# Performance work log

Hardware: AMD Instinct MI355X
Metric: run time of the kernel (lower is better)

The kernel has to match this reference:

```python
import jax, jax.numpy as jnp
import numpy as np

B, T = 32, 64
INPUT_DIM, EMB, HA, HB, NUM_CLASS = 4894, 128, 128, 128, 1
D_IN = EMB + 1  # use_time=True appends scalar time feature


def gru_cell(x, h, Wih, Whh, bih, bhh):
    # torch nn.GRU cell semantics, gate order (r, z, n)
    gi = x @ Wih.T + bih
    gh = h @ Whh.T + bhh
    ir, iz, i_n = jnp.split(gi, 3, axis=-1)
    hr, hz, hn = jnp.split(gh, 3, axis=-1)
    r = jax.nn.sigmoid(ir + hr)
    z = jax.nn.sigmoid(iz + hz)
    n = jnp.tanh(i_n + r * hn)
    return (1.0 - z) * n + z * h


def setup_inputs():
    key = jax.random.key(0)
    ks = jax.random.split(key, 14)
    f32 = jnp.float32
    s = lambda k, sh, sc: (jax.random.normal(k, sh) * sc).astype(f32)
    return {
        "x": jax.random.uniform(ks[0], (B, T, INPUT_DIM), dtype=f32),
        "t": jax.random.uniform(ks[1], (B, T), dtype=f32),
        "lengths": jax.random.randint(ks[2], (B,), 1, T + 1),
        "W_emb": s(ks[3], (EMB, INPUT_DIM), 0.02),
        "Wih_a": s(ks[4], (3 * HA, D_IN), 0.05),
        "Whh_a": s(ks[5], (3 * HA, HA), 0.05),
        "bih_a": jnp.zeros((3 * HA,), f32),
        "bhh_a": jnp.zeros((3 * HA,), f32),
        "Wih_b": s(ks[6], (3 * HB, D_IN), 0.05),
        "Whh_b": s(ks[7], (3 * HB, HB), 0.05),
        "bih_b": jnp.zeros((3 * HB,), f32),
        "bhh_b": jnp.zeros((3 * HB,), f32),
        "w_alpha": s(ks[8], (1, HA), 0.1),
        "b_alpha": jnp.zeros((1,), f32),
        "W_beta": s(ks[9], (EMB, HB), 0.1),
        "b_beta": jnp.zeros((EMB,), f32),
        "W_out": s(ks[10], (NUM_CLASS, EMB), 0.1),
        "b_out": jnp.zeros((NUM_CLASS,), f32),
    }


def reference(x, t, lengths, W_emb, Wih_a, Whh_a, bih_a, bhh_a,
              Wih_b, Whh_b, bih_b, bhh_b, w_alpha, b_alpha,
              W_beta, b_beta, W_out, b_out):
    # embedding (dropout is identity in inference)
    emb = x @ W_emb.T                                   # [B,T,E]
    temb = jnp.concatenate([emb, t[..., None]], axis=-1)  # [B,T,E+1]

    # reversed-prefix tensor: R[b,i,k] = temb[b, i-k] for k<=i else 0
    i_idx = jnp.arange(T)[:, None]
    k_idx = jnp.arange(T)[None, :]
    src = i_idx - k_idx                                  # [T,T]
    valid = (src >= 0)
    src_c = jnp.clip(src, 0)
    vmask = valid[None, :, :, None].astype(emb.dtype)
    R = jnp.take(temb, src_c, axis=1) * vmask            # [B,T,T,D_IN]
    E_rev = jnp.take(emb, src_c, axis=1) * vmask         # [B,T,T,E]

    # run alpha/beta GRUs along the prefix axis k (causal, so zero padding
    # at k>i never affects the k<=i outputs that we keep)
    R_k = jnp.moveaxis(R, 2, 0)                          # [Tk,B,T,D_IN]
    h0a = jnp.zeros((B, T, HA), emb.dtype)
    h0b = jnp.zeros((B, T, HB), emb.dtype)

    def step(carry, xk):
        ha, hb = carry
        ha = gru_cell(xk, ha, Wih_a, Whh_a, bih_a, bhh_a)
        hb = gru_cell(xk, hb, Wih_b, Whh_b, bih_b, bhh_b)
        return (ha, hb), (ha, hb)

    _, (Ha, Hb) = jax.lax.scan(step, (h0a, h0b), R_k)
    Ha = jnp.moveaxis(Ha, 0, 2)                          # [B,T,Tk,HA]
    Hb = jnp.moveaxis(Hb, 0, 2)                          # [B,T,Tk,HB]

    # attention over the i+1 prefix positions
    scores = (Ha @ w_alpha.T + b_alpha)[..., 0]          # [B,T,Tk]
    scores = jnp.where(valid[None], scores, jnp.float32(-1e9))
    alpha = jax.nn.softmax(scores, axis=-1)
    beta = jnp.tanh(Hb @ W_beta.T + b_beta)              # [B,T,Tk,E]

    c = jnp.einsum('btk,btke,btke->bte', alpha, beta, E_rev)
    row_valid = (jnp.arange(T)[None, :] < lengths[:, None]).astype(c.dtype)
    c = c * row_valid[..., None]                         # zero where i >= lengths[b]

    logits = c @ W_out.T + b_out                         # [B,T,1]
    return logits[..., 0]
```

## Files before the change

### kernel.cpp

```cpp
#include <hip/hip_runtime.h>
#include <hip/hip_bf16.h>

#define DEVI __device__ __forceinline__

typedef __attribute__((ext_vector_type(8))) short short8;
typedef __attribute__((ext_vector_type(8))) unsigned short ushort8;
typedef __attribute__((ext_vector_type(2))) unsigned int u32x2;
typedef __attribute__((ext_vector_type(4))) float f32x4;

static constexpr int TT = 64, KIN = 4894, KINP = 4896, E = 128;
static constexpr float L2E = 1.4426950408889634f;

DEVI unsigned short f2bf(float f) {
    union { float f; unsigned u; } v; v.f = f;
    unsigned r = v.u + 0x7fffu + ((v.u >> 16) & 1u);
    return (unsigned short)(r >> 16);
}
DEVI float sigm2(float x) { return __builtin_amdgcn_rcpf(1.f + __builtin_amdgcn_exp2f(-x)); }
DEVI float tanh2(float x) { return 1.f - 2.f * __builtin_amdgcn_rcpf(__builtin_amdgcn_exp2f(x + x) + 1.f); }

DEVI void gload16(const float* g, float* l) {
    __builtin_amdgcn_global_load_lds(
        (const __attribute__((address_space(1))) void*)g,
        (__attribute__((address_space(3))) void*)l, 16, 0, 0);
}

DEVI short8 cvt8(const float* __restrict__ p, float s) {
    float2 v0 = *(const float2*)p, v1 = *(const float2*)(p + 2);
    float2 v2 = *(const float2*)(p + 4), v3 = *(const float2*)(p + 6);
    short8 r;
    r[0] = (short)f2bf(v0.x * s); r[1] = (short)f2bf(v0.y * s);
    r[2] = (short)f2bf(v1.x * s); r[3] = (short)f2bf(v1.y * s);
    r[4] = (short)f2bf(v2.x * s); r[5] = (short)f2bf(v2.y * s);
    r[6] = (short)f2bf(v3.x * s); r[7] = (short)f2bf(v3.y * s);
    return r;
}
DEVI short8 cvt8pk(const float* __restrict__ p) {
    float2 v0 = *(const float2*)p, v1 = *(const float2*)(p + 2);
    float2 v2 = *(const float2*)(p + 4), v3 = *(const float2*)(p + 6);
    union { unsigned u[4]; short8 s; } o;
    asm("v_cvt_pk_bf16_f32 %0, %1, %2" : "=v"(o.u[0]) : "v"(v0.x), "v"(v0.y));
    asm("v_cvt_pk_bf16_f32 %0, %1, %2" : "=v"(o.u[1]) : "v"(v1.x), "v"(v1.y));
    asm("v_cvt_pk_bf16_f32 %0, %1, %2" : "=v"(o.u[2]) : "v"(v2.x), "v"(v2.y));
    asm("v_cvt_pk_bf16_f32 %0, %1, %2" : "=v"(o.u[3]) : "v"(v3.x), "v"(v3.y));
    return o.s;
}

__global__ void prep_kernel(const float* __restrict__ Wemb,
                            const float* __restrict__ Wih_a, const float* __restrict__ Wih_b,
                            const float* __restrict__ Whh_a, const float* __restrict__ Whh_b,
                            const float* __restrict__ Wbeta,
                            unsigned short* __restrict__ wembbf, unsigned short* __restrict__ wihbf,
                            unsigned short* __restrict__ whhbf, unsigned short* __restrict__ wbetabf) {
    int job = blockIdx.x * blockDim.x + threadIdx.x;
    const int JWE = 128 * 612, JWIH = 768 * 16, JWHH = 768 * 16, JWB = 128 * 16;
    if (job < JWE) {
        int row = job / 612, c8 = (job % 612) * 8;
        ushort8 v;
        #pragma unroll
        for (int jj = 0; jj < 8; ++jj) { int c = c8 + jj; v[jj] = (c < KIN) ? f2bf(Wemb[(long)row * KIN + c]) : (unsigned short)0; }
        *(ushort8*)(wembbf + (long)row * KINP + c8) = v;
        return;
    }
    job -= JWE;
    if (job < JWIH) {
        int g = job / 16, c8 = (job % 16) * 8;
        const float* src = (g < 384) ? (Wih_a + (long)g * 129) : (Wih_b + (long)(g - 384) * 129);
        ushort8 v;
        #pragma unroll
        for (int jj = 0; jj < 8; ++jj) v[jj] = f2bf(src[c8 + jj] * L2E);
        *(ushort8*)(wihbf + (long)g * 128 + c8) = v;
        return;
    }
    job -= JWIH;
    if (job < JWHH) {
        int g = job / 16, c8 = (job % 16) * 8;
        const float* src = (g < 384) ? (Whh_a + (long)g * 128) : (Whh_b + (long)(g - 384) * 128);
        ushort8 v;
        #pragma unroll
        for (int jj = 0; jj < 8; ++jj) v[jj] = f2bf(src[c8 + jj] * L2E);
        *(ushort8*)(whhbf + (long)g * 128 + c8) = v;
        return;
    }
    job -= JWHH;
    if (job < JWB) {
        int e = job / 16, c8 = (job % 16) * 8;
        ushort8 v;
        #pragma unroll
        for (int jj = 0; jj < 8; ++jj) v[jj] = f2bf(Wbeta[(long)e * 128 + c8 + jj] * L2E);
        *(ushort8*)(wbetabf + (long)e * 128 + c8) = v;
    }
}

__global__ __launch_bounds__(256) void emb_gemm(const float* __restrict__ x,
                                                const unsigned short* __restrict__ wembbf,
                                                float* __restrict__ pout) {
    const int ks = blockIdx.x & 3, m0 = (blockIdx.x >> 2) * 16;
    const int w = threadIdx.x >> 6, l = threadIdx.x & 63, lr = l & 15, lo = l >> 4;
    const int n0 = (2 * w) * 16 + lr, n1 = (2 * w + 1) * 16 + lr;
    const float* xrow = x + (long)(m0 + lr) * KIN;
    const int k0 = ks * 1216;
    f32x4 acc0 = {0, 0, 0, 0}, acc1 = {0, 0, 0, 0};
    #pragma unroll 2
    for (int kt = 0; kt < 38; ++kt) {
        int k = k0 + kt * 32 + lo * 8;
        short8 a = cvt8pk(xrow + k);
        short8 b0 = *(const short8*)(wembbf + (long)n0 * KINP + k);
        short8 b1 = *(const short8*)(wembbf + (long)n1 * KINP + k);
        acc0 = __builtin_amdgcn_mfma_f32_16x16x32_bf16(a, b0, acc0, 0, 0, 0);
        acc1 = __builtin_amdgcn_mfma_f32_16x16x32_bf16(a, b1, acc1, 0, 0, 0);
    }
    if (ks == 3) {
        int k = 4864 + lo * 8;
        short8 a;
        #pragma unroll
        for (int jj = 0; jj < 8; ++jj) { int c = k + jj; a[jj] = (c < KIN) ? (short)f2bf(xrow[c]) : (short)0; }
        short8 b0 = *(const short8*)(wembbf + (long)n0 * KINP + k);
        short8 b1 = *(const short8*)(wembbf + (long)n1 * KINP + k);
        acc0 = __builtin_amdgcn_mfma_f32_16x16x32_bf16(a, b0, acc0, 0, 0, 0);
        acc1 = __builtin_amdgcn_mfma_f32_16x16x32_bf16(a, b1, acc1, 0, 0, 0);
    }
    float* pbase = pout + (long)ks * 2048 * E;
    #pragma unroll
    for (int r = 0; r < 4; ++r) {
        int m = m0 + lo * 4 + r;
        pbase[(long)m * E + n0] = acc0[r];
        pbase[(long)m * E + n1] = acc1[r];
    }
}

__global__ __launch_bounds__(256) void gi_gemm(const float* __restrict__ pout,
                                               const unsigned short* __restrict__ wihbf,
                                               const float* __restrict__ Wih_a, const float* __restrict__ Wih_b,
                                               const float* __restrict__ t,
                                               const float* __restrict__ bih_a, const float* __restrict__ bih_b,
                                               const float* __restrict__ bhh_a, const float* __restrict__ bhh_b,
                                               const float* __restrict__ Wout,
                                               float* __restrict__ emb_swz_wo, float* __restrict__ Gi3) {
    const int m0 = blockIdx.x * 16;
    const int tid = threadIdx.x;
    const int w = tid >> 6, l = tid & 63, lr = l & 15, lo = l >> 4;
    __shared__ __align__(16) unsigned short embs[16][128];

    {
        const int trow = tid >> 4, e0 = (tid & 15) * 8;
        const int tok = m0 + trow;
        const long base = (long)tok * E + e0;
        f32x4 s0 = *(const f32x4*)(pout + base);
        f32x4 s1 = *(const f32x4*)(pout + base + 4);
        #pragma unroll
        for (int ks = 1; ks < 4; ++ks) {
            f32x4 v0 = *(const f32x4*)(pout + (long)ks * 2048 * E + base);
            f32x4 v1 = *(const f32x4*)(pout + (long)ks * 2048 * E + base + 4);
            #pragma unroll
            for (int jj = 0; jj < 4; ++jj) { s0[jj] += v0[jj]; s1[jj] += v1[jj]; }
        }
        ushort8 h;
        #pragma unroll
        for (int jj = 0; jj < 4; ++jj) { h[jj] = f2bf(s0[jj]); h[4 + jj] = f2bf(s1[jj]); }
        *(ushort8*)(&embs[trow][e0]) = h;
        f32x4 wo0 = *(const f32x4*)(Wout + e0);
        f32x4 wo1 = *(const f32x4*)(Wout + e0 + 4);
        #pragma unroll
        for (int jj = 0; jj < 4; ++jj) { s0[jj] *= wo0[jj]; s1[jj] *= wo1[jj]; }
        const int cc = (tok >> 6) & 15;
        const int x0 = e0 ^ ((cc & 7) << 2), x1 = (e0 + 4) ^ ((cc & 7) << 2);
        *(f32x4*)(emb_swz_wo + (long)tok * E + x0) = s0;
        *(f32x4*)(emb_swz_wo + (long)tok * E + x1) = s1;
    }
    __syncthreads();

    f32x4 acc[12];
    #pragma unroll
    for (int nl = 0; nl < 12; ++nl) acc[nl] = (f32x4){0, 0, 0, 0};
    #pragma unroll
    for (int kt = 0; kt < 4; ++kt) {
        int k = kt * 32 + lo * 8;
        short8 a0 = *(const short8*)(&embs[lr][k]);
        #pragma unroll
        for (int nl = 0; nl < 12; ++nl) {
            int n = (w * 12 + nl) * 16 + lr;
            short8 bf = *(const short8*)(wihbf + (long)n * 128 + k);
            acc[nl] = __builtin_amdgcn_mfma_f32_16x16x32_bf16(a0, bf, acc[nl], 0, 0, 0);
        }
    }
    #pragma unroll
    for (int nl = 0; nl < 12; ++nl) {
        int n = (w * 12 + nl) * 16 + lr;
        int gru = (n >= 384) ? 1 : 0;
        int nn = n - gru * 384;
        int gt = nn >> 7, u = nn & 127;
        float bias = (gru ? bih_b[nn] : bih_a[nn]);
        if (gt < 2) bias += (gru ? bhh_b[nn] : bhh_a[nn]);
        float cw = (n < 384) ? Wih_a[(long)n * 129 + 128] : Wih_b[(long)(n - 384) * 129 + 128];
        #pragma unroll
        for (int r = 0; r < 4; ++r) {
            int tok = m0 + lo * 4 + r;
            int cc = (tok >> 6) & 15;
            Gi3[(((long)tok * 2 + gru) * 3 + gt) * 128 + (u ^ ((cc & 7) << 2))] =
                acc[nl][r] + (bias + t[tok] * cw) * L2E;
        }
    }
}

__global__ __launch_bounds__(512, 1)
void retain_rec(const unsigned short* __restrict__ whhbf, const unsigned short* __restrict__ wbetabf,
                const float* __restrict__ Gi3, const float* __restrict__ emb_swz_wo,
                const float* __restrict__ bhh_a, const float* __restrict__ bhh_b,
                const float* __restrict__ w_alpha, const float* __restrict__ b_alpha,
                const float* __restrict__ b_beta,
                float* __restrict__ p_g, float* __restrict__ d_g) {
    const int tid = threadIdx.x;
    const int w = tid >> 6, l = tid & 63, lr = l & 15, lo = l >> 4;
    const int i = blockIdx.x >> 2, q = (blockIdx.x >> 1) & 1, g = blockIdx.x & 1;
    const int u0 = w * 16 + lo * 4;
    const int sw2 = (lr & 7) << 2;
    const int cS = tid >> 5, chk = tid & 31;

    __shared__ __align__(16) float Gst[3][3][16][128];
    __shared__ __align__(16) float Est[3][16][128];
    __shared__ __align__(16) unsigned short Hbf[2][16][128];
    __shared__ __align__(16) unsigned short Mld[2][16][128];
    __shared__ float pd_s[16][66];

    for (int idx = tid; idx < 2 * 16 * 128; idx += 512) (&Hbf[0][0][0])[idx] = 0;

    short8 Wf[3][4];
    #pragma unroll
    for (int gt = 0; gt < 3; ++gt)
        #pragma unroll
        for (int kt = 0; kt < 4; ++kt)
            Wf[gt][kt] = *(const short8*)(whhbf + (long)(g * 384 + gt * 128 + w * 16 + lr) * 128 + kt * 32 + lo * 8);
    short8 Xf[4];
    #pragma unroll
    for (int kt = 0; kt < 4; ++kt)
        Xf[kt] = g ? *(const short8*)(wbetabf + (long)(w * 16 + lr) * 128 + kt * 32 + lo * 8)
                   : cvt8(w_alpha + kt * 32 + lo * 8, L2E);
    short8 ones;
    #pragma unroll
    for (int jj = 0; jj < 8; ++jj) ones[jj] = (short)0x3F80;

    const float* bhhG = g ? bhh_b : bhh_a;
    f32x4 bhn4 = *(const f32x4*)(bhhG + 256 + u0);
    #pragma unroll
    for (int r = 0; r < 4; ++r) bhn4[r] *= L2E;
    f32x4 bb4 = {0, 0, 0, 0};
    if (g) {
        bb4 = *(const f32x4*)(b_beta + u0);
        #pragma unroll
        for (int r = 0; r < 4; ++r) bb4[r] *= L2E;
    }
    const float balL = b_alpha[0] * L2E;

    float h_old[4] = {0, 0, 0, 0};

    const long chainBase = (long)((q * 16 + cS) * 64);
    auto STAGE = [&](int b, int jg, int je) {
        const float* gb = Gi3 + ((chainBase + jg) * 2 + g) * 384 + chk * 4;
        gload16(gb,        (float*)&Gst[b][0][0][0] + (w << 8));
        gload16(gb + 128,  (float*)&Gst[b][1][0][0] + (w << 8));
        gload16(gb + 256,  (float*)&Gst[b][2][0][0] + (w << 8));
        if (g) gload16(emb_swz_wo + ((chainBase + je) << 7) + chk * 4, (float*)&Est[b][0][0] + (w << 8));
    };

    STAGE(0, i, (i + 1 > 63) ? 63 : i + 1);
    STAGE(1, (i - 1 < 0) ? 0 : i - 1, i);
    if (g) asm volatile("s_waitcnt lgkmcnt(0) vmcnt(4)" ::: "memory");
    else   asm volatile("s_waitcnt lgkmcnt(0) vmcnt(3)" ::: "memory");
    __builtin_amdgcn_s_barrier();
    __builtin_amdgcn_sched_barrier(0);

    const int iend = i + 1 + g;
    for (int n = 0; n <= iend; ++n) {
        const int bufc = n % 3, bufs = (n + 2) % 3;
        const int rb = n & 1, wb = rb ^ 1;
        const bool do_gate = (n <= i);
        const bool do_post = (n >= 1) && (n <= i + 1);

        {
            int jg = i - n - 2; if (jg < 0) jg = 0;
            int je = i - n - 1; if (je < 0) je = 0;
            STAGE(bufs, jg, je);
        }

        if (g && w == 0 && n >= 2) {
            f32x4 dacc = {0, 0, 0, 0};
            #pragma unroll
            for (int kt = 0; kt < 4; ++kt) {
                int sw = (kt * 32 + lo * 8) ^ ((lr & 7) * 8);
                short8 bm = *(const short8*)(&Mld[wb][lr][sw]);
                dacc = __builtin_amdgcn_mfma_f32_16x16x32_bf16(ones, bm, dacc, 0, 0, 0);
            }
            if (lo == 0) pd_s[lr][n - 2] = dacc[0];
        }

        short8 Af[4];
        if (do_gate || do_post) {
            #pragma unroll
            for (int kt = 0; kt < 4; ++kt) {
                int sw = (kt * 32 + lo * 8) ^ ((lr & 7) * 8);
                Af[kt] = *(const short8*)(&Hbf[rb][lr][sw]);
            }
        }

        f32x4 gh0 = {0, 0, 0, 0}, gh1 = {0, 0, 0, 0}, gh2 = bhn4;
        if (do_gate) {
            f32x4 a0 = {0, 0, 0, 0}, a1 = {0, 0, 0, 0}, a2 = {0, 0, 0, 0};
            #pragma unroll
            for (int kt = 0; kt < 2; ++kt) {
                gh0 = __builtin_amdgcn_mfma_f32_16x16x32_bf16(Wf[0][kt], Af[kt], gh0, 0, 0, 0);
                gh1 = __builtin_amdgcn_mfma_f32_16x16x32_bf16(Wf[1][kt], Af[kt], gh1, 0, 0, 0);
                gh2 = __builtin_amdgcn_mfma_f32_16x16x32_bf16(Wf[2][kt], Af[kt], gh2, 0, 0, 0);
                a0 = __builtin_amdgcn_mfma_f32_16x16x32_bf16(Wf[0][kt + 2], Af[kt + 2], a0, 0, 0, 0);
                a1 = __builtin_amdgcn_mfma_f32_16x16x32_bf16(Wf[1][kt + 2], Af[kt + 2], a1, 0, 0, 0);
                a2 = __builtin_amdgcn_mfma_f32_16x16x32_bf16(Wf[2][kt + 2], Af[kt + 2], a2, 0, 0, 0);
            }
            #pragma unroll
            for (int r = 0; r < 4; ++r) { gh0[r] += a0[r]; gh1[r] += a1[r]; gh2[r] += a2[r]; }
        }

        if (do_post) {
            f32x4 xacc = {0, 0, 0, 0}, xb = {0, 0, 0, 0};
            #pragma unroll
            for (int kt = 0; kt < 2; ++kt) {
                xacc = __builtin_amdgcn_mfma_f32_16x16x32_bf16(Xf[kt], Af[kt], xacc, 0, 0, 0);
                xb   = __builtin_amdgcn_mfma_f32_16x16x32_bf16(Xf[kt + 2], Af[kt + 2], xb, 0, 0, 0);
            }
            #pragma unroll
            for (int r = 0; r < 4; ++r) xacc[r] += xb[r];
            if (!g) {
                if (w == 0 && lo == 0) pd_s[lr][n - 1] = __builtin_amdgcn_exp2f(xacc[0] + balL);
            } else {
                f32x4 ew4 = *(const f32x4*)(&Est[bufc][lr][u0 ^ sw2]);
                float m0v = tanh2(xacc[0] + bb4[0]) * ew4[0];
                float m1v = tanh2(xacc[1] + bb4[1]) * ew4[1];
                float m2v = tanh2(xacc[2] + bb4[2]) * ew4[2];
                float m3v = tanh2(xacc[3] + bb4[3]) * ew4[3];
                unsigned mp0, mp1;
                asm("v_cvt_pk_bf16_f32 %0, %1, %2" : "=v"(mp0) : "v"(m0v), "v"(m1v));
                asm("v_cvt_pk_bf16_f32 %0, %1, %2" : "=v"(mp1) : "v"(m2v), "v"(m3v));
                *(u32x2*)(&Mld[rb][lr][u0 ^ ((lr & 7) * 8)]) = (u32x2){mp0, mp1};
            }
        }

        if (do_gate) {
            f32x4 gr = *(const f32x4*)(&Gst[bufc][0][lr][u0 ^ sw2]);
            f32x4 gz = *(const f32x4*)(&Gst[bufc][1][lr][u0 ^ sw2]);
            f32x4 gn = *(const f32x4*)(&Gst[bufc][2][lr][u0 ^ sw2]);
            float hn[4];
            #pragma unroll
            for (int r = 0; r < 4; ++r) {
                float rr = sigm2(gr[r] + gh0[r]);
                float zz = sigm2(gz[r] + gh1[r]);
                float nv = tanh2(gn[r] + rr * gh2[r]);
                float h = nv + zz * (h_old[r] - nv);
                h_old[r] = h;
                hn[r] = h;
            }
            unsigned p0, p1;
            asm("v_cvt_pk_bf16_f32 %0, %1, %2" : "=v"(p0) : "v"(hn[0]), "v"(hn[1]));
            asm("v_cvt_pk_bf16_f32 %0, %1, %2" : "=v"(p1) : "v"(hn[2]), "v"(hn[3]));
            *(u32x2*)(&Hbf[wb][lr][u0 ^ ((lr & 7) * 8)]) = (u32x2){p0, p1};
        }

        if (g) asm volatile("s_waitcnt lgkmcnt(0) vmcnt(4)" ::: "memory");
        else   asm volatile("s_waitcnt lgkmcnt(0) vmcnt(3)" ::: "memory");
        __builtin_amdgcn_s_barrier();
        __builtin_amdgcn_sched_barrier(0);
    }

    __syncthreads();

    float* dst = g ? d_g : p_g;
    for (int idx = tid; idx < 16 * 64; idx += 512) {
        int c = idx >> 6, kk = idx & 63;
        if (kk <= i) {
            long row = (long)(q * 16 + c) * 64 + i;
            dst[row * 64 + kk] = pd_s[c][kk];
        }
    }
}

__global__ __launch_bounds__(512) void reduce_out(const float* __restrict__ p_g, const float* __restrict__ d_g,
                                                  const int* __restrict__ lengths, const float* __restrict__ b_out,
                                                  float* __restrict__ out) {
    const int w = threadIdx.x >> 6, l = threadIdx.x & 63;
    const int row = blockIdx.x * 8 + w;
    const int b = row >> 6, i = row & 63;
    float p = (l <= i) ? p_g[(long)row * 64 + l] : 0.f;
    float d = (l <= i) ? d_g[(long)row * 64 + l] : 0.f;
    float pd = p * d;
    #pragma unroll
    for (int off = 1; off < 64; off <<= 1) {
        p += __shfl_xor(p, off);
        pd += __shfl_xor(pd, off);
    }
    if (l == 0) {
        float val = (i < lengths[b]) ? pd / p + b_out[0] : b_out[0];
        out[row] = val;
    }
}

extern "C" void kernel_launch(void* const* d_in, const int* in_sizes, int n_in,
                              void* d_out, int out_size, void* d_ws, size_t ws_size,
                              hipStream_t stream) {
    (void)in_sizes; (void)n_in; (void)out_size; (void)ws_size;
    const float* x       = (const float*)d_in[0];
    const float* t       = (const float*)d_in[1];
    const int*   len     = (const int*)d_in[2];
    const float* Wemb    = (const float*)d_in[3];
    const float* Wih_a   = (const float*)d_in[4];
    const float* Whh_a   = (const float*)d_in[5];
    const float* bih_a   = (const float*)d_in[6];
    const float* bhh_a   = (const float*)d_in[7];
    const float* Wih_b   = (const float*)d_in[8];
    const float* Whh_b   = (const float*)d_in[9];
    const float* bih_b   = (const float*)d_in[10];
    const float* bhh_b   = (const float*)d_in[11];
    const float* w_alpha = (const float*)d_in[12];
    const float* b_alpha = (const float*)d_in[13];
    const float* W_beta  = (const float*)d_in[14];
    const float* b_beta  = (const float*)d_in[15];
    const float* W_out   = (const float*)d_in[16];
    const float* b_out   = (const float*)d_in[17];

    char* ws = (char*)d_ws;
    float*          emb_swz = (float*)(ws + 0);
    float*          Gi3     = (float*)(ws + 1048576);
    unsigned short* wembbf  = (unsigned short*)(ws + 7340032);
    unsigned short* wihbf   = (unsigned short*)(ws + 8593408);
    unsigned short* whhbf   = (unsigned short*)(ws + 8790016);
    unsigned short* wbetabf = (unsigned short*)(ws + 8986624);
    float*          p_g     = (float*)(ws + 9019392);
    float*          d_g     = (float*)(ws + 9543680);
    float*          pout    = (float*)(ws + 10067968);

    const int jobs = 128 * 612 + 768 * 16 + 768 * 16 + 128 * 16;
    prep_kernel<<<(jobs + 255) / 256, 256, 0, stream>>>(Wemb, Wih_a, Wih_b, Whh_a, Whh_b, W_beta,
                                                        wembbf, wihbf, whhbf, wbetabf);
    emb_gemm<<<512, 256, 0, stream>>>(x, wembbf, pout);
    gi_gemm<<<128, 256, 0, stream>>>(pout, wihbf, Wih_a, Wih_b, t, bih_a, bih_b, bhh_a, bhh_b,
                                     W_out, emb_swz, Gi3);
    retain_rec<<<256, 512, 0, stream>>>(whhbf, wbetabf, Gi3, emb_swz, bhh_a, bhh_b,
                                        w_alpha, b_alpha, b_beta, p_g, d_g);
    reduce_out<<<256, 512, 0, stream>>>(p_g, d_g, len, b_out, (float*)d_out);
}
```

Measured before the change: 134.4 us.

## Halve recurrence block to 4 waves, double-buffer staging, and deepen emb split-K

```diff
diff --git a/kernel.cpp b/kernel.cpp
--- a/kernel.cpp
+++ b/kernel.cpp
@@ -95,14 +95,14 @@
 __global__ __launch_bounds__(256) void emb_gemm(const float* __restrict__ x,
                                                 const unsigned short* __restrict__ wembbf,
                                                 float* __restrict__ pout) {
-    const int ks = blockIdx.x & 3, m0 = (blockIdx.x >> 2) * 16;
+    const int ks = blockIdx.x & 7, m0 = (blockIdx.x >> 3) * 16;
     const int w = threadIdx.x >> 6, l = threadIdx.x & 63, lr = l & 15, lo = l >> 4;
     const int n0 = (2 * w) * 16 + lr, n1 = (2 * w + 1) * 16 + lr;
     const float* xrow = x + (long)(m0 + lr) * KIN;
-    const int k0 = ks * 1216;
+    const int k0 = ks * 608;
     f32x4 acc0 = {0, 0, 0, 0}, acc1 = {0, 0, 0, 0};
     #pragma unroll 2
-    for (int kt = 0; kt < 38; ++kt) {
+    for (int kt = 0; kt < 19; ++kt) {
         int k = k0 + kt * 32 + lo * 8;
         short8 a = cvt8pk(xrow + k);
         short8 b0 = *(const short8*)(wembbf + (long)n0 * KINP + k);
@@ -110,7 +110,7 @@
         acc0 = __builtin_amdgcn_mfma_f32_16x16x32_bf16(a, b0, acc0, 0, 0, 0);
         acc1 = __builtin_amdgcn_mfma_f32_16x16x32_bf16(a, b1, acc1, 0, 0, 0);
     }
-    if (ks == 3) {
+    if (ks == 7) {
         int k = 4864 + lo * 8;
         short8 a;
         #pragma unroll
@@ -149,7 +149,7 @@
         f32x4 s0 = *(const f32x4*)(pout + base);
         f32x4 s1 = *(const f32x4*)(pout + base + 4);
         #pragma unroll
-        for (int ks = 1; ks < 4; ++ks) {
+        for (int ks = 1; ks < 8; ++ks) {
             f32x4 v0 = *(const f32x4*)(pout + (long)ks * 2048 * E + base);
             f32x4 v1 = *(const f32x4*)(pout + (long)ks * 2048 * E + base + 4);
             #pragma unroll
@@ -203,7 +203,7 @@
     }
 }
 
-__global__ __launch_bounds__(512, 1)
+__global__ __launch_bounds__(256, 1)
 void retain_rec(const unsigned short* __restrict__ whhbf, const unsigned short* __restrict__ wbetabf,
                 const float* __restrict__ Gi3, const float* __restrict__ emb_swz_wo,
                 const float* __restrict__ bhh_a, const float* __restrict__ bhh_b,
@@ -213,81 +213,89 @@
     const int tid = threadIdx.x;
     const int w = tid >> 6, l = tid & 63, lr = l & 15, lo = l >> 4;
     const int i = blockIdx.x >> 2, q = (blockIdx.x >> 1) & 1, g = blockIdx.x & 1;
-    const int u0 = w * 16 + lo * 4;
+    const int u0a = w * 32 + lo * 4, u0b = u0a + 16;
     const int sw2 = (lr & 7) << 2;
+    const int bsw = (lr & 7) * 8;
     const int cS = tid >> 5, chk = tid & 31;
 
-    __shared__ __align__(16) float Gst[3][3][16][128];
-    __shared__ __align__(16) float Est[3][16][128];
+    __shared__ __align__(16) float Gst[2][3][16][128];
+    __shared__ __align__(16) float Est[2][16][128];
     __shared__ __align__(16) unsigned short Hbf[2][16][128];
     __shared__ __align__(16) unsigned short Mld[2][16][128];
     __shared__ float pd_s[16][66];
 
-    for (int idx = tid; idx < 2 * 16 * 128; idx += 512) (&Hbf[0][0][0])[idx] = 0;
-
-    short8 Wf[3][4];
-    #pragma unroll
-    for (int gt = 0; gt < 3; ++gt)
+    for (int idx = tid; idx < 2 * 16 * 128; idx += 256) (&Hbf[0][0][0])[idx] = 0;
+
+    short8 Wf[6][4];
+    #pragma unroll
+    for (int ut = 0; ut < 2; ++ut)
+        #pragma unroll
+        for (int gt = 0; gt < 3; ++gt)
+            #pragma unroll
+            for (int kt = 0; kt < 4; ++kt)
+                Wf[ut * 3 + gt][kt] = *(const short8*)(whhbf +
+                    (long)(g * 384 + gt * 128 + w * 32 + ut * 16 + lr) * 128 + kt * 32 + lo * 8);
+    short8 Xf[2][4];
+    #pragma unroll
+    for (int ut = 0; ut < 2; ++ut)
         #pragma unroll
         for (int kt = 0; kt < 4; ++kt)
-            Wf[gt][kt] = *(const short8*)(whhbf + (long)(g * 384 + gt * 128 + w * 16 + lr) * 128 + kt * 32 + lo * 8);
-    short8 Xf[4];
-    #pragma unroll
-    for (int kt = 0; kt < 4; ++kt)
-        Xf[kt] = g ? *(const short8*)(wbetabf + (long)(w * 16 + lr) * 128 + kt * 32 + lo * 8)
-                   : cvt8(w_alpha + kt * 32 + lo * 8, L2E);
+            Xf[ut][kt] = g ? *(const short8*)(wbetabf + (long)(w * 32 + ut * 16 + lr) * 128 + kt * 32 + lo * 8)
+                           : cvt8(w_alpha + kt * 32 + lo * 8, L2E);
     short8 ones;
     #pragma unroll
     for (int jj = 0; jj < 8; ++jj) ones[jj] = (short)0x3F80;
 
     const float* bhhG = g ? bhh_b : bhh_a;
-    f32x4 bhn4 = *(const f32x4*)(bhhG + 256 + u0);
-    #pragma unroll
-    for (int r = 0; r < 4; ++r) bhn4[r] *= L2E;
-    f32x4 bb4 = {0, 0, 0, 0};
+    f32x4 bhn4a = *(const f32x4*)(bhhG + 256 + u0a);
+    f32x4 bhn4b = *(const f32x4*)(bhhG + 256 + u0b);
+    #pragma unroll
+    for (int r = 0; r < 4; ++r) { bhn4a[r] *= L2E; bhn4b[r] *= L2E; }
+    f32x4 bb4a = {0, 0, 0, 0}, bb4b = {0, 0, 0, 0};
     if (g) {
-        bb4 = *(const f32x4*)(b_beta + u0);
-        #pragma unroll
-        for (int r = 0; r < 4; ++r) bb4[r] *= L2E;
+        bb4a = *(const f32x4*)(b_beta + u0a);
+        bb4b = *(const f32x4*)(b_beta + u0b);
+        #pragma unroll
+        for (int r = 0; r < 4; ++r) { bb4a[r] *= L2E; bb4b[r] *= L2E; }
     }
     const float balL = b_alpha[0] * L2E;
 
-    float h_old[4] = {0, 0, 0, 0};
-
-    const long chainBase = (long)((q * 16 + cS) * 64);
+    float h_old[2][4] = {{0, 0, 0, 0}, {0, 0, 0, 0}};
+
     auto STAGE = [&](int b, int jg, int je) {
-        const float* gb = Gi3 + ((chainBase + jg) * 2 + g) * 384 + chk * 4;
-        gload16(gb,        (float*)&Gst[b][0][0][0] + (w << 8));
-        gload16(gb + 128,  (float*)&Gst[b][1][0][0] + (w << 8));
-        gload16(gb + 256,  (float*)&Gst[b][2][0][0] + (w << 8));
-        if (g) gload16(emb_swz_wo + ((chainBase + je) << 7) + chk * 4, (float*)&Est[b][0][0] + (w << 8));
+        #pragma unroll
+        for (int h = 0; h < 2; ++h) {
+            const long cb = (long)((q * 16 + cS + 8 * h) * 64);
+            const float* gb = Gi3 + ((cb + jg) * 2 + g) * 384 + chk * 4;
+            const int dofs = (w << 8) + (h << 10);
+            gload16(gb,       (float*)&Gst[b][0][0][0] + dofs);
+            gload16(gb + 128, (float*)&Gst[b][1][0][0] + dofs);
+            gload16(gb + 256, (float*)&Gst[b][2][0][0] + dofs);
+            if (g) gload16(emb_swz_wo + ((cb + je) << 7) + chk * 4, (float*)&Est[b][0][0] + dofs);
+        }
     };
 
     STAGE(0, i, (i + 1 > 63) ? 63 : i + 1);
-    STAGE(1, (i - 1 < 0) ? 0 : i - 1, i);
-    if (g) asm volatile("s_waitcnt lgkmcnt(0) vmcnt(4)" ::: "memory");
-    else   asm volatile("s_waitcnt lgkmcnt(0) vmcnt(3)" ::: "memory");
-    __builtin_amdgcn_s_barrier();
-    __builtin_amdgcn_sched_barrier(0);
 
     const int iend = i + 1 + g;
     for (int n = 0; n <= iend; ++n) {
-        const int bufc = n % 3, bufs = (n + 2) % 3;
-        const int rb = n & 1, wb = rb ^ 1;
+        __syncthreads();
+
+        {
+            int jg = i - n - 1; if (jg < 0) jg = 0;
+            int je = i - n;     if (je < 0) je = 0;
+            STAGE((n + 1) & 1, jg, je);
+        }
+
+        const int rb = n & 1, wb = rb ^ 1, bufc = n & 1;
         const bool do_gate = (n <= i);
         const bool do_post = (n >= 1) && (n <= i + 1);
 
-        {
-            int jg = i - n - 2; if (jg < 0) jg = 0;
-            int je = i - n - 1; if (je < 0) je = 0;
-            STAGE(bufs, jg, je);
-        }
-
         if (g && w == 0 && n >= 2) {
             f32x4 dacc = {0, 0, 0, 0};
             #pragma unroll
             for (int kt = 0; kt < 4; ++kt) {
-                int sw = (kt * 32 + lo * 8) ^ ((lr & 7) * 8);
+                int sw = (kt * 32 + lo * 8) ^ bsw;
                 short8 bm = *(const short8*)(&Mld[wb][lr][sw]);
                 dacc = __builtin_amdgcn_mfma_f32_16x16x32_bf16(ones, bm, dacc, 0, 0, 0);
             }
@@ -298,81 +306,90 @@
         if (do_gate || do_post) {
             #pragma unroll
             for (int kt = 0; kt < 4; ++kt) {
-                int sw = (kt * 32 + lo * 8) ^ ((lr & 7) * 8);
+                int sw = (kt * 32 + lo * 8) ^ bsw;
                 Af[kt] = *(const short8*)(&Hbf[rb][lr][sw]);
             }
         }
 
-        f32x4 gh0 = {0, 0, 0, 0}, gh1 = {0, 0, 0, 0}, gh2 = bhn4;
+        f32x4 gh[6];
+        gh[0] = (f32x4){0, 0, 0, 0}; gh[1] = (f32x4){0, 0, 0, 0}; gh[2] = bhn4a;
+        gh[3] = (f32x4){0, 0, 0, 0}; gh[4] = (f32x4){0, 0, 0, 0}; gh[5] = bhn4b;
         if (do_gate) {
-            f32x4 a0 = {0, 0, 0, 0}, a1 = {0, 0, 0, 0}, a2 = {0, 0, 0, 0};
-            #pragma unroll
-            for (int kt = 0; kt < 2; ++kt) {
-                gh0 = __builtin_amdgcn_mfma_f32_16x16x32_bf16(Wf[0][kt], Af[kt], gh0, 0, 0, 0);
-                gh1 = __builtin_amdgcn_mfma_f32_16x16x32_bf16(Wf[1][kt], Af[kt], gh1, 0, 0, 0);
-                gh2 = __builtin_amdgcn_mfma_f32_16x16x32_bf16(Wf[2][kt], Af[kt], gh2, 0, 0, 0);
-                a0 = __builtin_amdgcn_mfma_f32_16x16x32_bf16(Wf[0][kt + 2], Af[kt + 2], a0, 0, 0, 0);
-                a1 = __builtin_amdgcn_mfma_f32_16x16x32_bf16(Wf[1][kt + 2], Af[kt + 2], a1, 0, 0, 0);
-                a2 = __builtin_amdgcn_mfma_f32_16x16x32_bf16(Wf[2][kt + 2], Af[kt + 2], a2, 0, 0, 0);
-            }
-            #pragma unroll
-            for (int r = 0; r < 4; ++r) { gh0[r] += a0[r]; gh1[r] += a1[r]; gh2[r] += a2[r]; }
+            #pragma unroll
+            for (int kt = 0; kt < 4; ++kt)
+                #pragma unroll
+                for (int tt = 0; tt < 6; ++tt)
+                    gh[tt] = __builtin_amdgcn_mfma_f32_16x16x32_bf16(Wf[tt][kt], Af[kt], gh[tt], 0, 0, 0);
         }
 
         if (do_post) {
-            f32x4 xacc = {0, 0, 0, 0}, xb = {0, 0, 0, 0};
-            #pragma unroll
-            for (int kt = 0; kt < 2; ++kt) {
-                xacc = __builtin_amdgcn_mfma_f32_16x16x32_bf16(Xf[kt], Af[kt], xacc, 0, 0, 0);
-                xb   = __builtin_amdgcn_mfma_f32_16x16x32_bf16(Xf[kt + 2], Af[kt + 2], xb, 0, 0, 0);
-            }
-            #pragma unroll
-            for (int r = 0; r < 4; ++r) xacc[r] += xb[r];
             if (!g) {
-                if (w == 0 && lo == 0) pd_s[lr][n - 1] = __builtin_amdgcn_exp2f(xacc[0] + balL);
+                if (w == 0) {
+                    f32x4 xacc = {0, 0, 0, 0};
+                    #pragma unroll
+                    for (int kt = 0; kt < 4; ++kt)
+                        xacc = __builtin_amdgcn_mfma_f32_16x16x32_bf16(Xf[0][kt], Af[kt], xacc, 0, 0, 0);
+                    if (lo == 0) pd_s[lr][n - 1] = __builtin_amdgcn_exp2f(xacc[0] + balL);
+                }
             } else {
-                f32x4 ew4 = *(const f32x4*)(&Est[bufc][lr][u0 ^ sw2]);
-                float m0v = tanh2(xacc[0] + bb4[0]) * ew4[0];
-                float m1v = tanh2(xacc[1] + bb4[1]) * ew4[1];
-                float m2v = tanh2(xacc[2] + bb4[2]) * ew4[2];
-                float m3v = tanh2(xacc[3] + bb4[3]) * ew4[3];
-                unsigned mp0, mp1;
+                f32x4 xa = {0, 0, 0, 0}, xb = {0, 0, 0, 0};
+                #pragma unroll
+                for (int kt = 0; kt < 4; ++kt) {
+                    xa = __builtin_amdgcn_mfma_f32_16x16x32_bf16(Xf[0][kt], Af[kt], xa, 0, 0, 0);
+                    xb = __builtin_amdgcn_mfma_f32_16x16x32_bf16(Xf[1][kt], Af[kt], xb, 0, 0, 0);
+                }
+                f32x4 ewa = *(const f32x4*)(&Est[bufc][lr][u0a ^ sw2]);
+                f32x4 ewb = *(const f32x4*)(&Est[bufc][lr][u0b ^ sw2]);
+                float m0v = tanh2(xa[0] + bb4a[0]) * ewa[0];
+                float m1v = tanh2(xa[1] + bb4a[1]) * ewa[1];
+                float m2v = tanh2(xa[2] + bb4a[2]) * ewa[2];
+                float m3v = tanh2(xa[3] + bb4a[3]) * ewa[3];
+                float m4v = tanh2(xb[0] + bb4b[0]) * ewb[0];
+                float m5v = tanh2(xb[1] + bb4b[1]) * ewb[1];
+                float m6v = tanh2(xb[2] + bb4b[2]) * ewb[2];
+                float m7v = tanh2(xb[3] + bb4b[3]) * ewb[3];
+                unsigned mp0, mp1, mp2, mp3;
                 asm("v_cvt_pk_bf16_f32 %0, %1, %2" : "=v"(mp0) : "v"(m0v), "v"(m1v));
                 asm("v_cvt_pk_bf16_f32 %0, %1, %2" : "=v"(mp1) : "v"(m2v), "v"(m3v));
-                *(u32x2*)(&Mld[rb][lr][u0 ^ ((lr & 7) * 8)]) = (u32x2){mp0, mp1};
+                asm("v_cvt_pk_bf16_f32 %0, %1, %2" : "=v"(mp2) : "v"(m4v), "v"(m5v));
+                asm("v_cvt_pk_bf16_f32 %0, %1, %2" : "=v"(mp3) : "v"(m6v), "v"(m7v));
+                *(u32x2*)(&Mld[rb][lr][u0a ^ bsw]) = (u32x2){mp0, mp1};
+                *(u32x2*)(&Mld[rb][lr][u0b ^ bsw]) = (u32x2){mp2, mp3};
             }
         }
 
         if (do_gate) {
-            f32x4 gr = *(const f32x4*)(&Gst[bufc][0][lr][u0 ^ sw2]);
-            f32x4 gz = *(const f32x4*)(&Gst[bufc][1][lr][u0 ^ sw2]);
-            f32x4 gn = *(const f32x4*)(&Gst[bufc][2][lr][u0 ^ sw2]);
-            float hn[4];
-            #pragma unroll
-            for (int r = 0; r < 4; ++r) {
-                float rr = sigm2(gr[r] + gh0[r]);
-                float zz = sigm2(gz[r] + gh1[r]);
-                float nv = tanh2(gn[r] + rr * gh2[r]);
-                float h = nv + zz * (h_old[r] - nv);
-                h_old[r] = h;
-                hn[r] = h;
+            float hn[2][4];
+            #pragma unroll
+            for (int ut = 0; ut < 2; ++ut) {
+                const int u0 = ut ? u0b : u0a;
+                f32x4 gr = *(const f32x4*)(&Gst[bufc][0][lr][u0 ^ sw2]);
+                f32x4 gz = *(const f32x4*)(&Gst[bufc][1][lr][u0 ^ sw2]);
+                f32x4 gn = *(const f32x4*)(&Gst[bufc][2][lr][u0 ^ sw2]);
+                #pragma unroll
+                for (int r = 0; r < 4; ++r) {
+                    float rr = sigm2(gr[r] + gh[ut * 3 + 0][r]);
+                    float zz = sigm2(gz[r] + gh[ut * 3 + 1][r]);
+                    float nv = tanh2(gn[r] + rr * gh[ut * 3 + 2][r]);
+                    float h = nv + zz * (h_old[ut][r] - nv);
+                    h_old[ut][r] = h;
+                    hn[ut][r] = h;
+                }
             }
-            unsigned p0, p1;
-            asm("v_cvt_pk_bf16_f32 %0, %1, %2" : "=v"(p0) : "v"(hn[0]), "v"(hn[1]));
-            asm("v_cvt_pk_bf16_f32 %0, %1, %2" : "=v"(p1) : "v"(hn[2]), "v"(hn[3]));
-            *(u32x2*)(&Hbf[wb][lr][u0 ^ ((lr & 7) * 8)]) = (u32x2){p0, p1};
-        }
-
-        if (g) asm volatile("s_waitcnt lgkmcnt(0) vmcnt(4)" ::: "memory");
-        else   asm volatile("s_waitcnt lgkmcnt(0) vmcnt(3)" ::: "memory");
-        __builtin_amdgcn_s_barrier();
-        __builtin_amdgcn_sched_barrier(0);
+            unsigned p0, p1, p2, p3;
+            asm("v_cvt_pk_bf16_f32 %0, %1, %2" : "=v"(p0) : "v"(hn[0][0]), "v"(hn[0][1]));
+            asm("v_cvt_pk_bf16_f32 %0, %1, %2" : "=v"(p1) : "v"(hn[0][2]), "v"(hn[0][3]));
+            asm("v_cvt_pk_bf16_f32 %0, %1, %2" : "=v"(p2) : "v"(hn[1][0]), "v"(hn[1][1]));
+            asm("v_cvt_pk_bf16_f32 %0, %1, %2" : "=v"(p3) : "v"(hn[1][2]), "v"(hn[1][3]));
+            *(u32x2*)(&Hbf[wb][lr][u0a ^ bsw]) = (u32x2){p0, p1};
+            *(u32x2*)(&Hbf[wb][lr][u0b ^ bsw]) = (u32x2){p2, p3};
+        }
     }
 
     __syncthreads();
 
     float* dst = g ? d_g : p_g;
-    for (int idx = tid; idx < 16 * 64; idx += 512) {
+    for (int idx = tid; idx < 16 * 64; idx += 256) {
         int c = idx >> 6, kk = idx & 63;
         if (kk <= i) {
             long row = (long)(q * 16 + c) * 64 + i;
@@ -438,10 +455,10 @@
     const int jobs = 128 * 612 + 768 * 16 + 768 * 16 + 128 * 16;
     prep_kernel<<<(jobs + 255) / 256, 256, 0, stream>>>(Wemb, Wih_a, Wih_b, Whh_a, Whh_b, W_beta,
                                                         wembbf, wihbf, whhbf, wbetabf);
-    emb_gemm<<<512, 256, 0, stream>>>(x, wembbf, pout);
+    emb_gemm<<<1024, 256, 0, stream>>>(x, wembbf, pout);
     gi_gemm<<<128, 256, 0, stream>>>(pout, wihbf, Wih_a, Wih_b, t, bih_a, bih_b, bhh_a, bhh_b,
                                      W_out, emb_swz, Gi3);
-    retain_rec<<<256, 512, 0, stream>>>(whhbf, wbetabf, Gi3, emb_swz, bhh_a, bhh_b,
+    retain_rec<<<256, 256, 0, stream>>>(whhbf, wbetabf, Gi3, emb_swz, bhh_a, bhh_b,
                                         w_alpha, b_alpha, b_beta, p_g, d_g);
     reduce_out<<<256, 512, 0, stream>>>(p_g, d_g, len, b_out, (float*)d_out);
 }
```

Result: slower. 152.0 us (+13.1%).
